# Optimization experiments

Measured on AMD Instinct MI355X. Metric: run time of the kernel, lower is better.

## Reference

```python
import jax, jax.numpy as jnp
import numpy as np

N, F_IN, H, HEADS, C, E = 4096, 768, 512, 4, 32, 131072
DH = H // HEADS


def gcn_conv(x, W, b, src, dst):
    # PyG GCNConv: add self-loops, symmetric normalization, scatter-add aggregation
    h = x @ W                                   # [N, H_out]
    loop = jnp.arange(N)
    s = jnp.concatenate([src, loop])            # sources incl self-loops
    d = jnp.concatenate([dst, loop])            # targets incl self-loops
    deg = jax.ops.segment_sum(jnp.ones_like(d, dtype=h.dtype), d, num_segments=N)
    dinv = jnp.where(deg > 0, jax.lax.rsqrt(deg), 0.0)
    norm = dinv[s] * dinv[d]                    # [E+N]
    msg = h[s] * norm[:, None]                  # gather + scale
    out = jax.ops.segment_sum(msg, d, num_segments=N)  # scatter-add
    return out + b


def mha(x, in_w, in_b, out_w, out_b):
    # torch.nn.MultiheadAttention, batch=1, q=k=v=x, eval (no dropout)
    qkv = x @ in_w.T + in_b                     # [N, 3H]
    q, k, v = jnp.split(qkv, 3, axis=-1)
    q = q.reshape(N, HEADS, DH)
    k = k.reshape(N, HEADS, DH)
    v = v.reshape(N, HEADS, DH)
    scale = 1.0 / jnp.sqrt(jnp.asarray(DH, x.dtype))
    scores = jnp.einsum('nhd,mhd->hnm', q * scale, k)   # [HEADS, N, N]
    attn = jax.nn.softmax(scores, axis=-1)
    o = jnp.einsum('hnm,mhd->nhd', attn, v).reshape(N, H)
    return o @ out_w.T + out_b


def setup_inputs() -> dict:
    key = jax.random.key(0)
    ks = jax.random.split(key, 12)
    f32 = jnp.float32
    return {
        'x': jax.random.normal(ks[0], (N, F_IN), dtype=f32),
        'edge_index': jax.random.randint(ks[1], (2, E), 0, N, dtype=jnp.int64),
        'W1': jax.random.normal(ks[2], (F_IN, H), dtype=f32) * (1.0 / np.sqrt(F_IN)),
        'b1': jnp.zeros((H,), dtype=f32),
        'in_w': jax.random.normal(ks[3], (3 * H, H), dtype=f32) * (1.0 / np.sqrt(H)),
        'in_b': jnp.zeros((3 * H,), dtype=f32),
        'out_w': jax.random.normal(ks[4], (H, H), dtype=f32) * (1.0 / np.sqrt(H)),
        'out_b': jnp.zeros((H,), dtype=f32),
        'W2': jax.random.normal(ks[5], (H, H), dtype=f32) * (1.0 / np.sqrt(H)),
        'b2': jnp.zeros((H,), dtype=f32),
        'Wc': jax.random.normal(ks[6], (H, C), dtype=f32) * (1.0 / np.sqrt(H)),
        'bc': jnp.zeros((C,), dtype=f32),
    }


def reference(x, edge_index, W1, b1, in_w, in_b, out_w, out_b, W2, b2, Wc, bc):
    src, dst = edge_index[0], edge_index[1]
    h = jax.nn.relu(gcn_conv(x, W1, b1, src, dst))
    h = h + mha(h, in_w, in_b, out_w, out_b)      # residual; dropout is identity (eval)
    h = jax.nn.relu(gcn_conv(h, W2, b2, src, dst))
    return h @ Wc + bc                             # [N, C]
```

## Files before the change

### kernel.cpp

```cpp
#include <hip/hip_runtime.h>

typedef unsigned short u16;
typedef unsigned int u32;
typedef __attribute__((ext_vector_type(8))) short bf16x8;
typedef __attribute__((ext_vector_type(4))) short bf16x4;
typedef __attribute__((ext_vector_type(4))) float f32x4;
typedef __attribute__((ext_vector_type(16))) float f32x16;

__device__ __forceinline__ float b2f(u16 b){ u32 u = ((u32)b)<<16; float f; __builtin_memcpy(&f,&u,4); return f; }
__device__ __forceinline__ u16 f2b(float f){ u32 u; __builtin_memcpy(&u,&f,4); u32 r = (u + 0x7fffu + ((u>>16)&1u)) >> 16; return (u16)r; }
__device__ __forceinline__ u32 cvtpk(float lo, float hi){ u32 r; asm("v_cvt_pk_bf16_f32 %0, %1, %2" : "=v"(r) : "v"(lo), "v"(hi)); return r; }
__device__ __forceinline__ void pswap(u32 &a, u32 &b){ asm("v_permlane32_swap_b32 %0, %1" : "+v"(a), "+v"(b)); }
__device__ __forceinline__ void gload16(const u16* g, u16* l){
  __builtin_amdgcn_global_load_lds((const __attribute__((address_space(1))) void*)g,
                                   (__attribute__((address_space(3))) void*)l, 16, 0, 0);
}

__device__ __forceinline__ void conv_body(const float* __restrict__ in, u16* __restrict__ out, int b, int n){
  int i = (b*256 + threadIdx.x)*4;
  if (i + 3 < n){
    float4 v = *(const float4*)(in + i);
    bf16x4 o;
    o[0]=(short)f2b(v.x); o[1]=(short)f2b(v.y); o[2]=(short)f2b(v.z); o[3]=(short)f2b(v.w);
    *(bf16x4*)(out + i) = o;
  } else {
    for (; i<n; ++i) out[i]=f2b(in[i]);
  }
}
__global__ __launch_bounds__(256) void prep_k(const float* __restrict__ x, const float* __restrict__ inw,
    const float* __restrict__ outw, const float* __restrict__ W1, const float* __restrict__ W2,
    const float* __restrict__ Wc, const int* __restrict__ dst, int E,
    u16* __restrict__ Xb, u16* __restrict__ inWb, u16* __restrict__ outWb,
    u16* __restrict__ W1T, u16* __restrict__ W2T, u16* __restrict__ WcT, int* __restrict__ deg){
  __shared__ float tile[32][33];
  int b = blockIdx.x;
  if (b < 3072){ conv_body(x, Xb, b, 4096*768); return; }
  if (b < 3840){ conv_body(inw, inWb, b-3072, 1536*512); return; }
  if (b < 4096){ conv_body(outw, outWb, b-3840, 512*512); return; }
  if (b < 4752){
    const float* in; u16* out; int R, C, bx, by;
    if (b < 4480){ in=W1; out=W1T; R=768; C=512; int lb=b-4096; bx=lb&15; by=lb>>4; }
    else if (b < 4736){ in=W2; out=W2T; R=512; C=512; int lb=b-4480; bx=lb&15; by=lb>>4; }
    else { in=Wc; out=WcT; R=512; C=32; bx=0; by=b-4736; }
    int tx = threadIdx.x & 31, ty = threadIdx.x >> 5;
    int c0 = bx*32, r0 = by*32;
    #pragma unroll
    for (int k=0;k<4;++k){
      int r = r0 + ty + k*8, c = c0 + tx;
      if (r < R && c < C) tile[ty+k*8][tx] = in[(size_t)r*C + c];
    }
    __syncthreads();
    #pragma unroll
    for (int k=0;k<4;++k){
      int c = c0 + ty + k*8, r = r0 + tx;
      if (r < R && c < C) out[(size_t)c*R + r] = f2b(tile[tx][ty+k*8]);
    }
    return;
  }
  int e = (b-4752)*256 + threadIdx.x;
  if (e < E) atomicAdd(&deg[dst[e]], 1);
}

__global__ __launch_bounds__(256) void scan_k(const int* __restrict__ deg, int* __restrict__ row_ptr,
                                              int* __restrict__ cursor, float* __restrict__ dinv){
  __shared__ int lds[256];
  int t = threadIdx.x;
  int base = t*16;
  int cnt[16]; int s = 0;
  #pragma unroll
  for (int k=0;k<16;++k){
    int d = deg[base+k] + 1;
    cnt[k] = d - 1;
    s += d - 1;
    dinv[base+k] = 1.0f / sqrtf((float)d);
  }
  lds[t] = s; __syncthreads();
  for (int o=1;o<256;o<<=1){
    int v = (t>=o) ? lds[t-o] : 0;
    __syncthreads();
    lds[t] += v;
    __syncthreads();
  }
  int run = lds[t] - s;
  #pragma unroll
  for (int k=0;k<16;++k){ row_ptr[base+k] = run; cursor[base+k] = run; run += cnt[k]; }
  if (t == 255) row_ptr[4096] = run;
}
__global__ __launch_bounds__(256) void scatter_k(const int* __restrict__ src, const int* __restrict__ dst,
                                                 int* __restrict__ cursor, int* __restrict__ srcl, int E){
  int e = blockIdx.x*256 + threadIdx.x;
  if (e < E){
    int d = dst[e];
    int pos = atomicAdd(&cursor[d], 1);
    srcl[pos] = src[e];
  }
}

__global__ __launch_bounds__(128) void aggregate_k(const u16* __restrict__ H, const float* __restrict__ dinv,
                                                   const int* __restrict__ rp, const int* __restrict__ srcl,
                                                   const float* __restrict__ bias, u16* __restrict__ out){
  const int i = blockIdx.x, t = threadIdx.x;
  const float di = dinv[i];
  bf16x4 hv = *(const bf16x4*)(H + (size_t)i*512 + t*4);
  float wself = di*di;
  float a0 = b2f((u16)hv[0])*wself, a1 = b2f((u16)hv[1])*wself, a2 = b2f((u16)hv[2])*wself, a3 = b2f((u16)hv[3])*wself;
  int e0 = rp[i], e1 = rp[i+1];
  int e = e0;
  for (; e+1 < e1; e += 2){
    int s0 = srcl[e], s1 = srcl[e+1];
    float w0 = dinv[s0]*di, w1 = dinv[s1]*di;
    bf16x4 v0 = *(const bf16x4*)(H + (size_t)s0*512 + t*4);
    bf16x4 v1 = *(const bf16x4*)(H + (size_t)s1*512 + t*4);
    a0 += b2f((u16)v0[0])*w0; a1 += b2f((u16)v0[1])*w0; a2 += b2f((u16)v0[2])*w0; a3 += b2f((u16)v0[3])*w0;
    a0 += b2f((u16)v1[0])*w1; a1 += b2f((u16)v1[1])*w1; a2 += b2f((u16)v1[2])*w1; a3 += b2f((u16)v1[3])*w1;
  }
  if (e < e1){
    int s = srcl[e];
    float w = dinv[s]*di;
    bf16x4 v = *(const bf16x4*)(H + (size_t)s*512 + t*4);
    a0 += b2f((u16)v[0])*w; a1 += b2f((u16)v[1])*w; a2 += b2f((u16)v[2])*w; a3 += b2f((u16)v[3])*w;
  }
  a0 += bias[t*4+0]; a1 += bias[t*4+1]; a2 += bias[t*4+2]; a3 += bias[t*4+3];
  a0 = fmaxf(a0,0.f); a1 = fmaxf(a1,0.f); a2 = fmaxf(a2,0.f); a3 = fmaxf(a3,0.f);
  bf16x4 o; o[0]=(short)f2b(a0); o[1]=(short)f2b(a1); o[2]=(short)f2b(a2); o[3]=(short)f2b(a3);
  *(bf16x4*)(out + (size_t)i*512 + t*4) = o;
}

template<int BM,int BN,int WM,int WN,bool BIAS,bool RESID,bool RELU,bool OUTBF,bool QKV>
__global__ __launch_bounds__(256) void gemm_abt_k(
    const u16* __restrict__ A, const u16* __restrict__ B,
    const float* __restrict__ bias, const u16* __restrict__ resid,
    u16* __restrict__ vt, void* __restrict__ Cp, int M, int N, int K)
{
  constexpr int BK = 64;
  constexpr int AISS = (BM*BK)/(256*8);
  constexpr int BISS = (BN*BK)/(256*8);
  constexpr int WC = BN/WN;
  constexpr int FM = WM/16, FN = WN/16;
  constexpr float QS = 0.088388347648318447f * 1.4426950408889634f;
  __shared__ u16 As[BM*BK];
  __shared__ u16 Bs[BN*BK];
  const int tid = threadIdx.x;
  const int wv = tid>>6, ln = tid&63;
  const int l15 = ln&15, l4 = ln>>4;
  const int wm = wv / WC, wn = wv % WC;
  const int bm0 = blockIdx.x*BM, bn0 = blockIdx.y*BN;
  const int arow = tid>>3;
  const int acol = (tid&7)*8;
  f32x4 acc[FM][FN];
  #pragma unroll
  for (int a=0;a<FM;++a)
    #pragma unroll
    for (int b=0;b<FN;++b) acc[a][b] = f32x4{0.f,0.f,0.f,0.f};
  for (int kt=0; kt<K; kt+=BK){
    #pragma unroll
    for (int i=0;i<AISS;++i) gload16(A + (size_t)(bm0 + i*32 + arow)*K + kt + acol, &As[i*2048 + wv*512]);
    #pragma unroll
    for (int i=0;i<BISS;++i) gload16(B + (size_t)(bn0 + i*32 + arow)*K + kt + acol, &Bs[i*2048 + wv*512]);
    __syncthreads();
    #pragma unroll
    for (int kc=0;kc<2;++kc){
      bf16x8 af[FM], bfr[FN];
      #pragma unroll
      for (int a=0;a<FM;++a) af[a] = *(const bf16x8*)(&As[(wm*WM + a*16 + l15)*BK + kc*32 + l4*8]);
      #pragma unroll
      for (int b=0;b<FN;++b) bfr[b] = *(const bf16x8*)(&Bs[(wn*WN + b*16 + l15)*BK + kc*32 + l4*8]);
      #pragma unroll
      for (int a=0;a<FM;++a)
        #pragma unroll
        for (int b=0;b<FN;++b)
          acc[a][b] = __builtin_amdgcn_mfma_f32_16x16x32_bf16(af[a], bfr[b], acc[a][b], 0,0,0);
    }
    __syncthreads();
  }
  #pragma unroll
  for (int a=0;a<FM;++a)
    #pragma unroll
    for (int b=0;b<FN;++b){
      int r0 = bm0 + wm*WM + a*16 + l4*4;
      int c  = bn0 + wn*WN + b*16 + l15;
      if constexpr (QKV){
        float v0 = acc[a][b][0] + bias[c];
        float v1 = acc[a][b][1] + bias[c];
        float v2 = acc[a][b][2] + bias[c];
        float v3 = acc[a][b][3] + bias[c];
        if (c >= 1024){
          bf16x4 pk; pk[0]=(short)f2b(v0); pk[1]=(short)f2b(v1); pk[2]=(short)f2b(v2); pk[3]=(short)f2b(v3);
          *(bf16x4*)(vt + (size_t)(c-1024)*4096 + r0) = pk;
        } else {
          float s = (c < 512) ? QS : 1.0f;
          u16* o = (u16*)Cp;
          o[(size_t)(r0+0)*N + c] = f2b(v0*s);
          o[(size_t)(r0+1)*N + c] = f2b(v1*s);
          o[(size_t)(r0+2)*N + c] = f2b(v2*s);
          o[(size_t)(r0+3)*N + c] = f2b(v3*s);
        }
      } else {
        #pragma unroll
        for (int j=0;j<4;++j){
          int r = r0 + j;
          float v = acc[a][b][j];
          if (BIAS)  v += bias[c];
          if (RESID) v += b2f(resid[(size_t)r*N + c]);
          if (RELU)  v = fmaxf(v, 0.f);
          if (OUTBF) ((u16*)Cp)[(size_t)r*N + c] = f2b(v);
          else       ((float*)Cp)[(size_t)r*N + c] = v;
        }
      }
    }
}

__global__ __launch_bounds__(256) void attn_k(const u16* __restrict__ qkv, const u16* __restrict__ vtg,
                                              u16* __restrict__ Op, float* __restrict__ Lp){
  __shared__ u16 Ks[64*128];
  __shared__ u16 Vs[128*128];
  const int head = blockIdx.y, split = blockIdx.z;
  const int qb0 = blockIdx.x*128;
  const int tid = threadIdx.x, wv = tid>>6, ln = tid&63;
  const int l31 = ln&31, hi = ln>>5;
  bf16x8 qf[8];
  {
    const u16* qp = qkv + (size_t)(qb0 + wv*32 + l31)*1536 + head*128 + hi*8;
    #pragma unroll
    for (int kk=0;kk<8;++kk) qf[kk] = *(const bf16x8*)(qp + kk*16);
  }
  f32x16 acc_o[4];
  #pragma unroll
  for (int d=0;d<4;++d)
    #pragma unroll
    for (int r=0;r<16;++r) acc_o[d][r] = 0.f;
  float l_part = 0.f;
  const int kR = ln, kG = wv*4;
  const int vR = tid>>1, vG = (tid&1)*4;
  const u16* kbase = qkv + 512 + (size_t)head*128;
  const u16* vbase = vtg + (size_t)(head*128 + vR)*4096;
  const int kv00 = split*1024;
  bf16x8 kreg[4], vreg[4];
  #pragma unroll
  for (int i=0;i<4;++i){
    kreg[i] = *(const bf16x8*)(kbase + (size_t)(kv00 + kR)*1536 + (kG+i)*8);
    vreg[i] = *(const bf16x8*)(vbase + kv00 + (vG+i)*8);
  }
  for (int it=0; it<16; ++it){
    #pragma unroll
    for (int i=0;i<4;++i){
      *(bf16x8*)((char*)Ks + kR*256 + (((kG+i)*16) ^ ((kR&15)<<4))) = kreg[i];
      *(bf16x8*)((char*)Vs + vR*256 + (((vG+i)*16) ^ ((vR&15)<<4))) = vreg[i];
    }
    __syncthreads();
    if (it < 15){
      int nb = kv00 + (it+1)*64;
      #pragma unroll
      for (int i=0;i<4;++i){
        kreg[i] = *(const bf16x8*)(kbase + (size_t)(nb + kR)*1536 + (kG+i)*8);
        vreg[i] = *(const bf16x8*)(vbase + nb + (vG+i)*8);
      }
    }
    f32x16 s0, s1;
    #pragma unroll
    for (int r=0;r<16;++r){ s0[r]=0.f; s1[r]=0.f; }
    #pragma unroll
    for (int kk=0;kk<8;++kk){
      int r0 = l31, r1 = 32 + l31;
      bf16x8 k0 = *(const bf16x8*)((char*)Ks + r0*256 + ((kk*32 + hi*16) ^ ((r0&15)<<4)));
      bf16x8 k1 = *(const bf16x8*)((char*)Ks + r1*256 + ((kk*32 + hi*16) ^ ((r1&15)<<4)));
      s0 = __builtin_amdgcn_mfma_f32_32x32x16_bf16(k0, qf[kk], s0, 0,0,0);
      s1 = __builtin_amdgcn_mfma_f32_32x32x16_bf16(k1, qf[kk], s1, 0,0,0);
    }
    union PU { u32 w[4]; bf16x8 v; };
    PU pa[4];
    #pragma unroll
    for (int g=0; g<2; ++g){
      float p[16];
      #pragma unroll
      for (int r=0;r<16;++r){ float sv = g ? s1[r] : s0[r]; p[r] = __builtin_amdgcn_exp2f(sv); l_part += p[r]; }
      u32 c0=cvtpk(p[0],p[1]), c1=cvtpk(p[2],p[3]), c2=cvtpk(p[4],p[5]), c3=cvtpk(p[6],p[7]);
      u32 c4=cvtpk(p[8],p[9]), c5=cvtpk(p[10],p[11]), c6=cvtpk(p[12],p[13]), c7=cvtpk(p[14],p[15]);
      pswap(c0,c2); pswap(c1,c3); pswap(c4,c6); pswap(c5,c7);
      pa[g*2+0].w[0]=c0; pa[g*2+0].w[1]=c1; pa[g*2+0].w[2]=c2; pa[g*2+0].w[3]=c3;
      pa[g*2+1].w[0]=c4; pa[g*2+1].w[1]=c5; pa[g*2+1].w[2]=c6; pa[g*2+1].w[3]=c7;
    }
    #pragma unroll
    for (int dg=0;dg<4;++dg){
      int row = dg*32 + l31;
      #pragma unroll
      for (int kvf=0;kvf<4;++kvf){
        bf16x8 vf = *(const bf16x8*)((char*)Vs + row*256 + ((kvf*32 + hi*16) ^ ((row&15)<<4)));
        acc_o[dg] = __builtin_amdgcn_mfma_f32_32x32x16_bf16(pa[kvf].v, vf, acc_o[dg], 0,0,0);
      }
    }
    __syncthreads();
  }
  float l_tot = l_part + __shfl_xor(l_part, 32, 64);
  if (hi == 0) Lp[split*4096 + qb0 + wv*32 + l31] = l_tot;
  #pragma unroll
  for (int dg=0;dg<4;++dg){
    #pragma unroll
    for (int r=0;r<16;++r){
      int q = qb0 + wv*32 + (r&3) + ((r>>2)<<3) + hi*4;
      Op[((size_t)split*4096 + q)*512 + head*128 + dg*32 + l31] = f2b(acc_o[dg][r]);
    }
  }
}

__global__ __launch_bounds__(256) void combine_k(const u16* __restrict__ Op, const float* __restrict__ Lp,
                                                 u16* __restrict__ oatt){
  int idx = blockIdx.x*256 + threadIdx.x;
  int n = idx >> 6, c8 = (idx & 63) << 3;
  float l = 0.f;
  #pragma unroll
  for (int s=0;s<4;++s) l += Lp[s*4096+n];
  float inv = 1.0f/l;
  float acc[8] = {0,0,0,0,0,0,0,0};
  #pragma unroll
  for (int s=0;s<4;++s){
    bf16x8 v = *(const bf16x8*)(Op + ((size_t)(s*4096+n))*512 + c8);
    #pragma unroll
    for (int j=0;j<8;++j) acc[j] += b2f((u16)v[j]);
  }
  bf16x8 o;
  #pragma unroll
  for (int j=0;j<8;++j) o[j] = (short)f2b(acc[j]*inv);
  *(bf16x8*)(oatt + (size_t)n*512 + c8) = o;
}

extern "C" void kernel_launch(void* const* d_in, const int* in_sizes, int n_in,
                              void* d_out, int out_size, void* d_ws, size_t ws_size,
                              hipStream_t stream) {
  (void)n_in; (void)out_size; (void)ws_size;
  const float* x    = (const float*)d_in[0];
  const int*   ei   = (const int*)d_in[1];
  const float* W1   = (const float*)d_in[2];
  const float* b1   = (const float*)d_in[3];
  const float* inw  = (const float*)d_in[4];
  const float* inb  = (const float*)d_in[5];
  const float* outw = (const float*)d_in[6];
  const float* outb = (const float*)d_in[7];
  const float* W2   = (const float*)d_in[8];
  const float* b2   = (const float*)d_in[9];
  const float* Wc   = (const float*)d_in[10];
  const float* bc   = (const float*)d_in[11];
  float* out = (float*)d_out;
  const int E = in_sizes[1] / 2;
  const int* srcp = ei;
  const int* dstp = ei + E;

  char* base = (char*)d_ws;
  size_t off = 0;
  auto alloc = [&](size_t bytes)->void*{
    void* p = base + off;
    off = (off + bytes + 255) & ~((size_t)255);
    return p;
  };
  u16* Xb    = (u16*)alloc((size_t)4096*768*2);
  u16* W1T   = (u16*)alloc((size_t)512*768*2);
  u16* inWb  = (u16*)alloc((size_t)1536*512*2);
  u16* outWb = (u16*)alloc((size_t)512*512*2);
  u16* W2T   = (u16*)alloc((size_t)512*512*2);
  u16* WcT   = (u16*)alloc((size_t)32*512*2);
  u16* Hpre  = (u16*)alloc((size_t)4096*512*2);
  u16* h1    = (u16*)alloc((size_t)4096*512*2);
  u16* qkvb  = (u16*)alloc((size_t)4096*1536*2);
  u16* vtg   = (u16*)alloc((size_t)512*4096*2);
  u16* oatt  = (u16*)alloc((size_t)4096*512*2);
  u16* h2    = (u16*)alloc((size_t)4096*512*2);
  u16* h3    = (u16*)alloc((size_t)4096*512*2);
  u16* Opart = (u16*)alloc((size_t)4*4096*512*2);
  float* Lpart = (float*)alloc((size_t)4*4096*4);
  int*   deg  = (int*)alloc(4096*4);
  float* dinv = (float*)alloc(4096*4);
  int*   rowp = (int*)alloc(4097*4);
  int*   curs = (int*)alloc(4096*4);
  int*   srcl = (int*)alloc((size_t)E*4);

  hipMemsetAsync(deg, 0, 4096*sizeof(int), stream);
  int degBlocks = (E + 255)/256;
  prep_k<<<4752 + degBlocks, 256, 0, stream>>>(x, inw, outw, W1, W2, Wc, dstp, E,
                                               Xb, inWb, outWb, W1T, W2T, WcT, deg);
  scan_k<<<1,256,0,stream>>>(deg, rowp, curs, dinv);
  scatter_k<<<(E+255)/256,256,0,stream>>>(srcp, dstp, curs, srcl, E);

  gemm_abt_k<128,64,64,32,false,false,false,true,false><<<dim3(32,8),256,0,stream>>>(Xb, W1T, nullptr, nullptr, nullptr, Hpre, 4096, 512, 768);
  aggregate_k<<<4096,128,0,stream>>>(Hpre, dinv, rowp, srcl, b1, h1);

  gemm_abt_k<128,64,64,32,true,false,false,true,true><<<dim3(32,24),256,0,stream>>>(h1, inWb, inb, nullptr, vtg, qkvb, 4096, 1536, 512);
  attn_k<<<dim3(32,4,4),256,0,stream>>>(qkvb, vtg, Opart, Lpart);
  combine_k<<<1024,256,0,stream>>>(Opart, Lpart, oatt);
  gemm_abt_k<128,64,64,32,true,true,false,true,false><<<dim3(32,8),256,0,stream>>>(oatt, outWb, outb, h1, nullptr, h2, 4096, 512, 512);

  gemm_abt_k<128,64,64,32,false,false,false,true,false><<<dim3(32,8),256,0,stream>>>(h2, W2T, nullptr, nullptr, nullptr, Hpre, 4096, 512, 512);
  aggregate_k<<<4096,128,0,stream>>>(Hpre, dinv, rowp, srcl, b2, h3);

  gemm_abt_k<64,32,16,32,true,false,false,false,false><<<dim3(64,1),256,0,stream>>>(h3, WcT, bc, nullptr, nullptr, out, 4096, 32, 512);
}
```

Baseline: 182.3 us.

## Unroll aggregation by four, keep attention partials in fp32, add attn occupancy hint

Unrolls the GCN neighbor gather loop from two to four edges per iteration so more independent loads are in flight. The split-K attention partial outputs are now stored as fp32 instead of bf16, and the combine kernel reads them with float4 loads. attn_k also gets a launch-bounds minimum of two blocks per CU, which may limit registers. Storing fp32 partials doubles that intermediate's memory traffic but drops a rounding step before the combine.

Result: faster. 173.9 us (-4.6%).

```diff
diff --git a/kernel.cpp b/kernel.cpp
--- a/kernel.cpp
+++ b/kernel.cpp
@@ -106,15 +106,19 @@
   float a0 = b2f((u16)hv[0])*wself, a1 = b2f((u16)hv[1])*wself, a2 = b2f((u16)hv[2])*wself, a3 = b2f((u16)hv[3])*wself;
   int e0 = rp[i], e1 = rp[i+1];
   int e = e0;
-  for (; e+1 < e1; e += 2){
-    int s0 = srcl[e], s1 = srcl[e+1];
-    float w0 = dinv[s0]*di, w1 = dinv[s1]*di;
+  for (; e+3 < e1; e += 4){
+    int s0 = srcl[e], s1 = srcl[e+1], s2 = srcl[e+2], s3 = srcl[e+3];
+    float w0 = dinv[s0]*di, w1 = dinv[s1]*di, w2 = dinv[s2]*di, w3 = dinv[s3]*di;
     bf16x4 v0 = *(const bf16x4*)(H + (size_t)s0*512 + t*4);
     bf16x4 v1 = *(const bf16x4*)(H + (size_t)s1*512 + t*4);
+    bf16x4 v2 = *(const bf16x4*)(H + (size_t)s2*512 + t*4);
+    bf16x4 v3 = *(const bf16x4*)(H + (size_t)s3*512 + t*4);
     a0 += b2f((u16)v0[0])*w0; a1 += b2f((u16)v0[1])*w0; a2 += b2f((u16)v0[2])*w0; a3 += b2f((u16)v0[3])*w0;
     a0 += b2f((u16)v1[0])*w1; a1 += b2f((u16)v1[1])*w1; a2 += b2f((u16)v1[2])*w1; a3 += b2f((u16)v1[3])*w1;
-  }
-  if (e < e1){
+    a0 += b2f((u16)v2[0])*w2; a1 += b2f((u16)v2[1])*w2; a2 += b2f((u16)v2[2])*w2; a3 += b2f((u16)v2[3])*w2;
+    a0 += b2f((u16)v3[0])*w3; a1 += b2f((u16)v3[1])*w3; a2 += b2f((u16)v3[2])*w3; a3 += b2f((u16)v3[3])*w3;
+  }
+  for (; e < e1; ++e){
     int s = srcl[e];
     float w = dinv[s]*di;
     bf16x4 v = *(const bf16x4*)(H + (size_t)s*512 + t*4);
@@ -210,8 +214,8 @@
     }
 }
 
-__global__ __launch_bounds__(256) void attn_k(const u16* __restrict__ qkv, const u16* __restrict__ vtg,
-                                              u16* __restrict__ Op, float* __restrict__ Lp){
+__global__ __launch_bounds__(256,2) void attn_k(const u16* __restrict__ qkv, const u16* __restrict__ vtg,
+                                                float* __restrict__ Op, float* __restrict__ Lp){
   __shared__ u16 Ks[64*128];
   __shared__ u16 Vs[128*128];
   const int head = blockIdx.y, split = blockIdx.z;
@@ -298,25 +302,25 @@
     #pragma unroll
     for (int r=0;r<16;++r){
       int q = qb0 + wv*32 + (r&3) + ((r>>2)<<3) + hi*4;
-      Op[((size_t)split*4096 + q)*512 + head*128 + dg*32 + l31] = f2b(acc_o[dg][r]);
-    }
-  }
-}
-
-__global__ __launch_bounds__(256) void combine_k(const u16* __restrict__ Op, const float* __restrict__ Lp,
+      Op[((size_t)split*4096 + q)*512 + head*128 + dg*32 + l31] = acc_o[dg][r];
+    }
+  }
+}
+
+__global__ __launch_bounds__(256) void combine_k(const float* __restrict__ Op, const float* __restrict__ Lp,
                                                  u16* __restrict__ oatt){
   int idx = blockIdx.x*256 + threadIdx.x;
   int n = idx >> 6, c8 = (idx & 63) << 3;
-  float l = 0.f;
-  #pragma unroll
-  for (int s=0;s<4;++s) l += Lp[s*4096+n];
+  float l = Lp[n] + Lp[4096+n] + Lp[8192+n] + Lp[12288+n];
   float inv = 1.0f/l;
   float acc[8] = {0,0,0,0,0,0,0,0};
   #pragma unroll
   for (int s=0;s<4;++s){
-    bf16x8 v = *(const bf16x8*)(Op + ((size_t)(s*4096+n))*512 + c8);
-    #pragma unroll
-    for (int j=0;j<8;++j) acc[j] += b2f((u16)v[j]);
+    const float* p = Op + ((size_t)(s*4096+n))*512 + c8;
+    float4 u = *(const float4*)p;
+    float4 v = *(const float4*)(p+4);
+    acc[0]+=u.x; acc[1]+=u.y; acc[2]+=u.z; acc[3]+=u.w;
+    acc[4]+=v.x; acc[5]+=v.y; acc[6]+=v.z; acc[7]+=v.w;
   }
   bf16x8 o;
   #pragma unroll
@@ -365,7 +369,7 @@
   u16* oatt  = (u16*)alloc((size_t)4096*512*2);
   u16* h2    = (u16*)alloc((size_t)4096*512*2);
   u16* h3    = (u16*)alloc((size_t)4096*512*2);
-  u16* Opart = (u16*)alloc((size_t)4*4096*512*2);
+  float* Opart = (float*)alloc((size_t)4*4096*512*4);
   float* Lpart = (float*)alloc((size_t)4*4096*4);
   int*   deg  = (int*)alloc(4096*4);
   float* dinv = (float*)alloc(4096*4);
```
